# Performance work log

Hardware: AMD Instinct MI355X
Metric: run time of the kernel (lower is better)

Reference implementation:

```python
import jax, jax.numpy as jnp
import numpy as np

BS, N, K = 64, 256, 64
IN_DIM, HID = 64, 64

def _mlp2(x, W1, b1, W2, b2, act_last):
    h = jax.nn.silu(x @ W1 + b1)
    h = h @ W2 + b2
    return jax.nn.silu(h) if act_last else h

def setup_inputs() -> dict:
    key = jax.random.key(0)
    ks = jax.random.split(key, 16)
    def g(k, shape, scale=1.0):
        return jax.random.normal(k, shape, dtype=jnp.float32) * scale
    s_e1 = 1.0 / np.sqrt(2 * IN_DIM + 1)
    s_h = 1.0 / np.sqrt(HID)
    s_h1 = 1.0 / np.sqrt(IN_DIM + HID)
    return {
        "ped_features": g(ks[0], (BS, N, 2)),
        "h_st": g(ks[1], (BS, N, IN_DIM)),
        "h_neigh": g(ks[2], (BS, N, K, IN_DIM)),
        "rela_features": g(ks[3], (BS, N, K, 6)),
        "neigh_mask": jax.random.bernoulli(ks[4], 0.7, (BS, N, K)),
        # f_e: Linear(2*in+1, hid), SiLU, Linear(hid, hid), SiLU
        "We1": g(ks[5], (2 * IN_DIM + 1, HID), s_e1), "be1": g(ks[6], (HID,), s_e1),
        "We2": g(ks[7], (HID, HID), s_h), "be2": g(ks[8], (HID,), s_h),
        # f_x: Linear(hid, hid), SiLU, Linear(hid, 1)
        "Wx1": g(ks[9], (HID, HID), s_h), "bx1": g(ks[10], (HID,), s_h),
        "Wx2": g(ks[11], (HID, 1), s_h), "bx2": g(ks[12], (1,), s_h),
        # f_h: Linear(in+hid, hid), SiLU, Linear(hid, hid)
        "Wh1": g(ks[13], (IN_DIM + HID, HID), s_h1), "bh1": g(ks[14], (HID,), s_h1),
        "Wh2": g(ks[15], (HID, HID), s_h), "bh2": g(jax.random.fold_in(key, 99), (HID,), s_h),
    }

def reference(ped_features, h_st, h_neigh, rela_features, neigh_mask,
              We1, be1, We2, be2, Wx1, bx1, Wx2, bx2, Wh1, bh1, Wh2, bh2):
    bs, n, k, _ = h_neigh.shape
    # pairwise distances from relative xy: [bs, N, k]
    dists = jnp.linalg.norm(rela_features[..., :2], axis=-1)
    neigh_num = neigh_mask.sum(axis=-1).astype(h_st.dtype)  # [bs, N]
    # broadcast h_st over neighbor axis and concat: [bs, N, k, 2*in+1]
    h_st_b = jnp.broadcast_to(h_st[:, :, None, :], (bs, n, k, h_st.shape[-1]))
    tmp = jnp.concatenate([h_st_b, h_neigh, dists[..., None]], axis=-1)
    m_ij = _mlp2(tmp, We1, be1, We2, be2, act_last=True)  # [bs, N, k, hid]
    m_ij = jnp.where(neigh_mask[..., None], m_ij, 0.0)
    gate = _mlp2(m_ij, Wx1, bx1, Wx2, bx2, act_last=False)  # [bs, N, k, 1]
    agg = (rela_features[..., :2] * gate).sum(axis=-2)  # [bs, N, 2]
    agg = agg / (neigh_num[..., None] + 1e-6)
    x_new = ped_features + agg
    m_i = m_ij.sum(axis=-2)  # [bs, N, hid]
    h_new = h_st + _mlp2(jnp.concatenate([h_st, m_i], axis=-1), Wh1, bh1, Wh2, bh2, act_last=False)
    return (x_new, h_new)
```

## Files before the change

### kernel.cpp

```cpp
#include <hip/hip_runtime.h>
#include <hip/hip_bf16.h>


typedef __attribute__((ext_vector_type(8))) short short8;
typedef __attribute__((ext_vector_type(4))) float f32x4;
typedef __attribute__((ext_vector_type(2))) float f32x2;
typedef __attribute__((ext_vector_type(2))) unsigned int u32x2;
typedef __attribute__((ext_vector_type(4))) unsigned int u32x4;

#define NODES 16384
#define NPB   16
#define NBLK  (NODES / NPB)

#define MFMA16(a, b, c) __builtin_amdgcn_mfma_f32_16x16x32_bf16((a), (b), (c), 0, 0, 0)

__device__ __forceinline__ unsigned short f2bf(float f) {
  unsigned int u = __float_as_uint(f);
  u += 0x7FFFu + ((u >> 16) & 1u);
  return (unsigned short)(u >> 16);
}
__device__ __forceinline__ unsigned int pk2(float lo, float hi) {
  unsigned int a = __float_as_uint(hi) + 0x8000u;
  unsigned int b = __float_as_uint(lo) + 0x8000u;
  return __builtin_amdgcn_perm(a, b, 0x07060302u);
}
__device__ __forceinline__ float bfl(unsigned int u) { return __uint_as_float(u << 16); }
__device__ __forceinline__ float bfh(unsigned int u) { return __uint_as_float(u & 0xFFFF0000u); }
__device__ __forceinline__ float silu_f(float x) {
  return x * __builtin_amdgcn_rcpf(1.f + __expf(-x));
}
__device__ __forceinline__ f32x4 silu4(f32x4 x) {
  f32x4 r; r[0]=silu_f(x[0]); r[1]=silu_f(x[1]); r[2]=silu_f(x[2]); r[3]=silu_f(x[3]); return r;
}
__device__ __forceinline__ short8 packb(f32x4 a, f32x4 b) {
  u32x4 t;
  t[0] = pk2(a[0], a[1]); t[1] = pk2(a[2], a[3]);
  t[2] = pk2(b[0], b[1]); t[3] = pk2(b[2], b[3]);
  return __builtin_bit_cast(short8, t);
}
__device__ __forceinline__ short8 ldfragT(const float* __restrict__ W, int k0, int col) {
  short8 r;
  #pragma unroll
  for (int m = 0; m < 8; m++) r[m] = (short)f2bf(W[(k0 + m) * 64 + col]);
  return r;
}

__global__ __launch_bounds__(256, 2) void egnn_mfma(
    const float* __restrict__ ped, const float* __restrict__ h_st,
    const float* __restrict__ h_neigh, const float* __restrict__ rela,
    const unsigned char* __restrict__ mask8,
    const float* __restrict__ We1, const float* __restrict__ be1,
    const float* __restrict__ We2, const float* __restrict__ be2,
    const float* __restrict__ Wx1, const float* __restrict__ bx1,
    const float* __restrict__ Wx2, const float* __restrict__ bx2,
    const float* __restrict__ Wh1, const float* __restrict__ bh1,
    const float* __restrict__ Wh2, const float* __restrict__ bh2,
    float* __restrict__ out)
{
  __shared__ __align__(16) float s_hst[16][64];
  __shared__ __align__(16) float s_u[16][64];
  __shared__ __align__(16) float s_miw[4][16][64];
  __shared__ __align__(16) unsigned int s_scr[4][16][40];
  __shared__ __align__(16) short8 s_af[16][64];
  __shared__ float s_cvec[2][64];
  __shared__ float s_w1l[64];
  __shared__ float s_wx2[64];
  __shared__ float s_aggx[4][16], s_aggy[4][16], s_nn[4][16];
  __shared__ int s_flags[2];

  const int t  = threadIdx.x;
  const int l  = t & 63;
  const int w  = t >> 6;
  const int lg = l >> 4;
  const int jl = l & 15;
  const int base = blockIdx.x * NPB;

  if (t == 0) { s_flags[0] = 1; s_flags[1] = 1; }
  __syncthreads();
  {
    const unsigned int* mw = (const unsigned int*)mask8;
    unsigned int iok = 1, fok = 1;
    #pragma unroll
    for (int q = 0; q < 4; q++) {
      unsigned int v = mw[t * 4 + q];
      if (v > 1u) iok = 0;
      if (v != 0u && v != 0x3F800000u) fok = 0;
    }
    if (!iok) atomicAnd(&s_flags[0], 0);
    if (!fok) atomicAnd(&s_flags[1], 0);
  }
  {
    const f32x4* src = (const f32x4*)(h_st + (size_t)base * 64);
    f32x4* dst = (f32x4*)&s_hst[0][0];
    dst[t] = src[t];
    if (t < 64)        s_cvec[0][t] = be2[t];
    else if (t < 128)  s_cvec[1][t - 64] = bx1[t - 64];
    else if (t < 192)  s_w1l[t - 128] = We1[128 * 64 + (t - 128)];
    else               s_wx2[t - 192] = Wx2[t - 192];
  }
  #pragma unroll
  for (int ci = 0; ci < 4; ci++) {
    const int c  = 4 * w + ci;
    const int g  = c >> 3, mt = (c >> 1) & 3, kk = c & 1;
    const float* W = g ? Wx1 : We2;
    s_af[c][l] = ldfragT(W, 8 * lg + 32 * kk, 16 * mt + jl);
  }
  __syncthreads();
  const int mode = s_flags[0] ? 0 : (s_flags[1] ? 1 : 2);

  auto ldmask = [&](size_t idx) -> float {
    if (mode == 0)      return (((const int*)mask8)[idx] != 0) ? 1.f : 0.f;
    else if (mode == 1) return (((const float*)mask8)[idx] != 0.f) ? 1.f : 0.f;
    else                return (mask8[idx] != 0) ? 1.f : 0.f;
  };

  {
    f32x4 uacc = {0.f, 0.f, 0.f, 0.f};
    #pragma unroll
    for (int kk = 0; kk < 2; kk++) {
      short8 au = ldfragT(We1, 8 * lg + 32 * kk, 16 * w + jl);
      f32x4 q0 = *(const f32x4*)&s_hst[jl][8 * lg + 32 * kk];
      f32x4 q1 = *(const f32x4*)&s_hst[jl][8 * lg + 32 * kk + 4];
      uacc = MFMA16(au, packb(q0, q1), uacc);
    }
    f32x4 b1v = *(const f32x4*)(be1 + 16 * w + 4 * lg);
    *(f32x4*)&s_u[jl][16 * w + 4 * lg] = uacc + b1v;
  }

  short8 a1[4][2];
  #pragma unroll
  for (int mt = 0; mt < 4; mt++)
    #pragma unroll
    for (int kk = 0; kk < 2; kk++)
      a1[mt][kk] = ldfragT(We1 + 64 * 64, 8 * lg + 32 * kk, 16 * mt + jl);
  const float bx2s = bx2[0];

  const float* hn_lane = h_neigh + ((size_t)base * 64 + 16 * w + jl) * 64 + 8 * lg;
  const size_t ro = (size_t)base * 64 + 16 * w + jl;
  f32x4 pf0 = *(const f32x4*)(hn_lane + 0);
  f32x4 pf1 = *(const f32x4*)(hn_lane + 4);
  f32x4 pf2 = *(const f32x4*)(hn_lane + 32);
  f32x4 pf3 = *(const f32x4*)(hn_lane + 36);
  f32x2 pre = *(const f32x2*)(rela + ro * 6);
  float pmf = ldmask(ro);
  __syncthreads();

  #pragma unroll 1
  for (int nl = 0; nl < NPB; nl++) {
    const short8 b1k0 = packb(pf0, pf1);
    const short8 b1k1 = packb(pf2, pf3);
    const f32x2 rr = pre; const float mf = pmf;
    if (nl < NPB - 1) {
      const float* p = hn_lane + (size_t)(nl + 1) * 4096;
      pf0 = *(const f32x4*)(p + 0);  pf1 = *(const f32x4*)(p + 4);
      pf2 = *(const f32x4*)(p + 32); pf3 = *(const f32x4*)(p + 36);
      pre = *(const f32x2*)(rela + (ro + (size_t)(nl + 1) * 64) * 6);
      pmf = ldmask(ro + (size_t)(nl + 1) * 64);
    }
    const float d = sqrtf(rr[0] * rr[0] + rr[1] * rr[1]);

    float msum = mf;
    msum += __shfl_xor(msum, 1, 64); msum += __shfl_xor(msum, 2, 64);
    msum += __shfl_xor(msum, 4, 64); msum += __shfl_xor(msum, 8, 64);
    if (l == 0) s_nn[w][nl] = msum;

    f32x4 acc[4];
    #pragma unroll
    for (int ht = 0; ht < 4; ht++) {
      const f32x4 wl = *(const f32x4*)&s_w1l[16 * ht + 4 * lg];
      acc[ht] = *(const f32x4*)&s_u[nl][16 * ht + 4 * lg] + d * wl;
      acc[ht] = MFMA16(a1[ht][0], b1k0, acc[ht]);
      acc[ht] = MFMA16(a1[ht][1], b1k1, acc[ht]);
    }
    #pragma unroll
    for (int ht = 0; ht < 4; ht++) {
      f32x4 e = silu4(acc[ht]);
      u32x2 wv; wv[0] = pk2(e[0], e[1]); wv[1] = pk2(e[2], e[3]);
      *(u32x2*)&s_scr[w][jl][8 * ht + 2 * lg] = wv;
    }
    short8 b2k0 = *(const short8*)&s_scr[w][jl][4 * lg];
    short8 b2k1 = *(const short8*)&s_scr[w][jl][16 + 4 * lg];

    #pragma unroll
    for (int ht = 0; ht < 4; ht++) {
      const short8 f2k0 = s_af[2 * ht][l];
      const short8 f2k1 = s_af[2 * ht + 1][l];
      acc[ht] = *(const f32x4*)&s_cvec[0][16 * ht + 4 * lg];
      acc[ht] = MFMA16(f2k0, b2k0, acc[ht]);
      acc[ht] = MFMA16(f2k1, b2k1, acc[ht]);
    }
    #pragma unroll
    for (int ht = 0; ht < 4; ht++) {
      f32x4 m = silu4(acc[ht]) * mf;
      u32x2 wv; wv[0] = pk2(m[0], m[1]); wv[1] = pk2(m[2], m[3]);
      *(u32x2*)&s_scr[w][jl][8 * ht + 2 * lg] = wv;
    }
    short8 b3k0 = *(const short8*)&s_scr[w][jl][4 * lg];
    short8 b3k1 = *(const short8*)&s_scr[w][jl][16 + 4 * lg];

    {
      const int hw = l & 31, jh = l >> 5;
      float pe = 0.f, po = 0.f;
      #pragma unroll
      for (int c = 0; c < 8; c++) {
        unsigned int v = s_scr[w][8 * jh + c][hw];
        pe += bfl(v); po += bfh(v);
      }
      pe += __shfl_xor(pe, 32, 64);
      po += __shfl_xor(po, 32, 64);
      if (l < 32) {
        f32x2 v2; v2[0] = pe; v2[1] = po;
        *(f32x2*)&s_miw[w][nl][2 * hw] = v2;
      }
    }

    #pragma unroll
    for (int ht = 0; ht < 4; ht++) {
      const short8 f3k0 = s_af[8 + 2 * ht][l];
      const short8 f3k1 = s_af[8 + 2 * ht + 1][l];
      acc[ht] = *(const f32x4*)&s_cvec[1][16 * ht + 4 * lg];
      acc[ht] = MFMA16(f3k0, b3k0, acc[ht]);
      acc[ht] = MFMA16(f3k1, b3k1, acc[ht]);
    }
    float gg = 0.f;
    #pragma unroll
    for (int ht = 0; ht < 4; ht++) {
      const f32x4 wx = *(const f32x4*)&s_wx2[16 * ht + 4 * lg];
      f32x4 g = silu4(acc[ht]);
      gg += g[0] * wx[0] + g[1] * wx[1] + g[2] * wx[2] + g[3] * wx[3];
    }
    gg += __shfl_xor(gg, 16, 64);
    gg += __shfl_xor(gg, 32, 64);
    const float gate = gg + bx2s;

    float ax = rr[0] * gate, ay = rr[1] * gate;
    ax += __shfl_xor(ax, 1, 64); ay += __shfl_xor(ay, 1, 64);
    ax += __shfl_xor(ax, 2, 64); ay += __shfl_xor(ay, 2, 64);
    ax += __shfl_xor(ax, 4, 64); ay += __shfl_xor(ay, 4, 64);
    ax += __shfl_xor(ax, 8, 64); ay += __shfl_xor(ay, 8, 64);
    if (l == 0) { s_aggx[w][nl] = ax; s_aggy[w][nl] = ay; }
  }
  __syncthreads();

  if (t < 32) {
    const int node = t >> 1, c = t & 1;
    const float nn = s_nn[0][node] + s_nn[1][node] + s_nn[2][node] + s_nn[3][node];
    const float ag = (c ? (s_aggy[0][node] + s_aggy[1][node] + s_aggy[2][node] + s_aggy[3][node])
                        : (s_aggx[0][node] + s_aggx[1][node] + s_aggx[2][node] + s_aggx[3][node]));
    out[(size_t)(base + node) * 2 + c] =
        ped[(size_t)(base + node) * 2 + c] + ag / (nn + 1e-6f);
  }

  {
    f32x4 hacc = *(const f32x4*)(bh1 + 16 * w + 4 * lg);
    #pragma unroll
    for (int kk = 0; kk < 4; kk++) {
      short8 ah = ldfragT(Wh1, 8 * lg + 32 * kk, 16 * w + jl);
      f32x4 q0, q1;
      if (kk < 2) {
        q0 = *(const f32x4*)&s_hst[jl][8 * lg + 32 * kk];
        q1 = *(const f32x4*)&s_hst[jl][8 * lg + 32 * kk + 4];
      } else {
        const int off = 8 * lg + 32 * (kk - 2);
        q0 = *(const f32x4*)&s_miw[0][jl][off]     + *(const f32x4*)&s_miw[1][jl][off]
           + *(const f32x4*)&s_miw[2][jl][off]     + *(const f32x4*)&s_miw[3][jl][off];
        q1 = *(const f32x4*)&s_miw[0][jl][off + 4] + *(const f32x4*)&s_miw[1][jl][off + 4]
           + *(const f32x4*)&s_miw[2][jl][off + 4] + *(const f32x4*)&s_miw[3][jl][off + 4];
      }
      hacc = MFMA16(ah, packb(q0, q1), hacc);
    }
    f32x4 h1 = silu4(hacc);
    u32x2 wv; wv[0] = pk2(h1[0], h1[1]); wv[1] = pk2(h1[2], h1[3]);
    *(u32x2*)&s_scr[0][jl][8 * w + 2 * lg] = wv;
  }
  __syncthreads();
  {
    short8 hb0 = *(const short8*)&s_scr[0][jl][4 * lg];
    short8 hb1 = *(const short8*)&s_scr[0][jl][16 + 4 * lg];
    short8 aw0 = ldfragT(Wh2, 8 * lg,      16 * w + jl);
    short8 aw1 = ldfragT(Wh2, 8 * lg + 32, 16 * w + jl);
    f32x4 oacc = *(const f32x4*)(bh2 + 16 * w + 4 * lg);
    oacc = MFMA16(aw0, hb0, oacc);
    oacc = MFMA16(aw1, hb1, oacc);
    f32x4 res = oacc + *(const f32x4*)&s_hst[jl][16 * w + 4 * lg];
    *(f32x4*)(out + 32768 + (size_t)(base + jl) * 64 + 16 * w + 4 * lg) = res;
  }
}

extern "C" void kernel_launch(void* const* d_in, const int* in_sizes, int n_in,
                              void* d_out, int out_size, void* d_ws, size_t ws_size,
                              hipStream_t stream) {
  (void)in_sizes; (void)n_in; (void)out_size; (void)d_ws; (void)ws_size;
  const float* ped     = (const float*)d_in[0];
  const float* h_st    = (const float*)d_in[1];
  const float* h_neigh = (const float*)d_in[2];
  const float* rela    = (const float*)d_in[3];
  const unsigned char* mask = (const unsigned char*)d_in[4];
  const float* We1 = (const float*)d_in[5];  const float* be1 = (const float*)d_in[6];
  const float* We2 = (const float*)d_in[7];  const float* be2 = (const float*)d_in[8];
  const float* Wx1 = (const float*)d_in[9];  const float* bx1 = (const float*)d_in[10];
  const float* Wx2 = (const float*)d_in[11]; const float* bx2 = (const float*)d_in[12];
  const float* Wh1 = (const float*)d_in[13]; const float* bh1 = (const float*)d_in[14];
  const float* Wh2 = (const float*)d_in[15]; const float* bh2 = (const float*)d_in[16];

  hipLaunchKernelGGL(egnn_mfma, dim3(NBLK), dim3(256), 0, stream,
                     ped, h_st, h_neigh, rela, mask,
                     We1, be1, We2, be2, Wx1, bx1, Wx2, bx2,
                     Wh1, bh1, Wh2, bh2, (float*)d_out);
}
```

Baseline: 117.5 us.

## Use hardware bf16 pack, re-layout LDS scratch, move gate MFMA before reduction

Replaces the manual bf16 round-and-permute packing with the v_cvt_pk_bf16_f32 instruction. Reorganizes the per-wave LDS scratch into a [half][lane][4] layout so each lane reads its B fragment contiguously, and rotates the reduction read order to avoid bank conflicts. Also moves the gate MLP MFMAs ahead of the m_i column reduction so matrix work can overlap the LDS reduction. The hardware convert rounds ties to even, while the old packing rounded ties away from zero, so results may differ slightly.

```diff
diff --git a/kernel.cpp b/kernel.cpp
--- a/kernel.cpp
+++ b/kernel.cpp
@@ -20,9 +20,9 @@
   return (unsigned short)(u >> 16);
 }
 __device__ __forceinline__ unsigned int pk2(float lo, float hi) {
-  unsigned int a = __float_as_uint(hi) + 0x8000u;
-  unsigned int b = __float_as_uint(lo) + 0x8000u;
-  return __builtin_amdgcn_perm(a, b, 0x07060302u);
+  unsigned int r;
+  asm("v_cvt_pk_bf16_f32 %0, %1, %2" : "=v"(r) : "v"(lo), "v"(hi));
+  return r;
 }
 __device__ __forceinline__ float bfl(unsigned int u) { return __uint_as_float(u << 16); }
 __device__ __forceinline__ float bfh(unsigned int u) { return __uint_as_float(u & 0xFFFF0000u); }
@@ -60,7 +60,7 @@
   __shared__ __align__(16) float s_hst[16][64];
   __shared__ __align__(16) float s_u[16][64];
   __shared__ __align__(16) float s_miw[4][16][64];
-  __shared__ __align__(16) unsigned int s_scr[4][16][40];
+  __shared__ __align__(16) unsigned int s_scr[4][2][64][4];
   __shared__ __align__(16) short8 s_af[16][64];
   __shared__ float s_cvec[2][64];
   __shared__ float s_w1l[64];
@@ -113,6 +113,9 @@
     else if (mode == 1) return (((const float*)mask8)[idx] != 0.f) ? 1.f : 0.f;
     else                return (mask8[idx] != 0) ? 1.f : 0.f;
   };
+
+  const int sc_lgp_e = (lg >> 1);
+  const int sc_m0    = 2 * (lg & 1);
 
   {
     f32x4 uacc = {0.f, 0.f, 0.f, 0.f};
@@ -176,10 +179,12 @@
     for (int ht = 0; ht < 4; ht++) {
       f32x4 e = silu4(acc[ht]);
       u32x2 wv; wv[0] = pk2(e[0], e[1]); wv[1] = pk2(e[2], e[3]);
-      *(u32x2*)&s_scr[w][jl][8 * ht + 2 * lg] = wv;
-    }
-    short8 b2k0 = *(const short8*)&s_scr[w][jl][4 * lg];
-    short8 b2k1 = *(const short8*)&s_scr[w][jl][16 + 4 * lg];
+      const int half = (4 * ht + lg) >> 3;
+      const int lgp  = (2 * ht + sc_lgp_e) & 3;
+      *(u32x2*)&s_scr[w][half][lgp * 16 + jl][sc_m0] = wv;
+    }
+    short8 b2k0 = *(const short8*)&s_scr[w][0][l][0];
+    short8 b2k1 = *(const short8*)&s_scr[w][1][l][0];
 
     #pragma unroll
     for (int ht = 0; ht < 4; ht++) {
@@ -193,17 +198,33 @@
     for (int ht = 0; ht < 4; ht++) {
       f32x4 m = silu4(acc[ht]) * mf;
       u32x2 wv; wv[0] = pk2(m[0], m[1]); wv[1] = pk2(m[2], m[3]);
-      *(u32x2*)&s_scr[w][jl][8 * ht + 2 * lg] = wv;
-    }
-    short8 b3k0 = *(const short8*)&s_scr[w][jl][4 * lg];
-    short8 b3k1 = *(const short8*)&s_scr[w][jl][16 + 4 * lg];
+      const int half = (4 * ht + lg) >> 3;
+      const int lgp  = (2 * ht + sc_lgp_e) & 3;
+      *(u32x2*)&s_scr[w][half][lgp * 16 + jl][sc_m0] = wv;
+    }
+    short8 b3k0 = *(const short8*)&s_scr[w][0][l][0];
+    short8 b3k1 = *(const short8*)&s_scr[w][1][l][0];
+
+    #pragma unroll
+    for (int ht = 0; ht < 4; ht++) {
+      const short8 f3k0 = s_af[8 + 2 * ht][l];
+      const short8 f3k1 = s_af[8 + 2 * ht + 1][l];
+      acc[ht] = *(const f32x4*)&s_cvec[1][16 * ht + 4 * lg];
+      acc[ht] = MFMA16(f3k0, b3k0, acc[ht]);
+      acc[ht] = MFMA16(f3k1, b3k1, acc[ht]);
+    }
 
     {
       const int hw = l & 31, jh = l >> 5;
+      const int half = hw >> 4;
+      const int lgp  = (hw & 15) >> 2;
+      const int m0   = hw & 3;
+      const int rot  = hw >> 2;
       float pe = 0.f, po = 0.f;
       #pragma unroll
       for (int c = 0; c < 8; c++) {
-        unsigned int v = s_scr[w][8 * jh + c][hw];
+        const int j = 8 * jh + ((c + rot) & 7);
+        unsigned int v = s_scr[w][half][lgp * 16 + j][m0];
         pe += bfl(v); po += bfh(v);
       }
       pe += __shfl_xor(pe, 32, 64);
@@ -214,14 +235,6 @@
       }
     }
 
-    #pragma unroll
-    for (int ht = 0; ht < 4; ht++) {
-      const short8 f3k0 = s_af[8 + 2 * ht][l];
-      const short8 f3k1 = s_af[8 + 2 * ht + 1][l];
-      acc[ht] = *(const f32x4*)&s_cvec[1][16 * ht + 4 * lg];
-      acc[ht] = MFMA16(f3k0, b3k0, acc[ht]);
-      acc[ht] = MFMA16(f3k1, b3k1, acc[ht]);
-    }
     float gg = 0.f;
     #pragma unroll
     for (int ht = 0; ht < 4; ht++) {
@@ -271,12 +284,14 @@
     }
     f32x4 h1 = silu4(hacc);
     u32x2 wv; wv[0] = pk2(h1[0], h1[1]); wv[1] = pk2(h1[2], h1[3]);
-    *(u32x2*)&s_scr[0][jl][8 * w + 2 * lg] = wv;
-  }
-  __syncthreads();
-  {
-    short8 hb0 = *(const short8*)&s_scr[0][jl][4 * lg];
-    short8 hb1 = *(const short8*)&s_scr[0][jl][16 + 4 * lg];
+    const int half = (4 * w + lg) >> 3;
+    const int lgp  = (2 * w + sc_lgp_e) & 3;
+    *(u32x2*)&s_scr[0][half][lgp * 16 + jl][sc_m0] = wv;
+  }
+  __syncthreads();
+  {
+    short8 hb0 = *(const short8*)&s_scr[0][0][l][0];
+    short8 hb1 = *(const short8*)&s_scr[0][1][l][0];
     short8 aw0 = ldfragT(Wh2, 8 * lg,      16 * w + jl);
     short8 aw1 = ldfragT(Wh2, 8 * lg + 32, 16 * w + jl);
     f32x4 oacc = *(const f32x4*)(bh2 + 16 * w + 4 * lg);
```

Result: faster. 111.9 us (-4.8%).
